# Optimization experiments

Hardware: AMD Instinct MI355X
Metric: run time of the kernel (lower is better)

The kernel has to match this reference:

```python
import jax, jax.numpy as jnp
import numpy as np

L = 3          # num encoder layers
H = 128        # hidden_dim
NH = 8         # num_heads
HD = H // NH   # head_dim
FF = H * 4     # ff inner dim (after GLU)
B, N = 32, 512
NUM_BINS = 50


def _linear_params(key, fan_in, fan_out):
    kw, kb = jax.random.split(key)
    lim = 1.0 / np.sqrt(fan_in)
    W = jax.random.uniform(kw, (fan_in, fan_out), jnp.float32, -lim, lim)
    b = jax.random.uniform(kb, (fan_out,), jnp.float32, -lim, lim)
    return W, b


def setup_inputs() -> dict:
    key = jax.random.key(0)
    ks = jax.random.split(key, 16)
    x = jax.random.normal(ks[0], (B, N, H), jnp.float32)
    distance_matrix = jax.random.uniform(ks[1], (B, N, N), jnp.float32)
    mask = jax.random.randint(ks[2], (B, N), 0, 2).astype(bool)

    def stack_linear(k, fan_in, fan_out):
        Ws, bs = [], []
        for l in range(L):
            W, b = _linear_params(jax.random.fold_in(k, l), fan_in, fan_out)
            Ws.append(W); bs.append(b)
        return jnp.stack(Ws), jnp.stack(bs)

    Wq, bq = stack_linear(ks[3], H, H)
    Wk, bk = stack_linear(ks[4], H, H)
    Wv, bv = stack_linear(ks[5], H, H)
    Wo, bo = stack_linear(ks[6], H, H)
    dist_emb = jax.random.normal(ks[7], (L, NUM_BINS, NH), jnp.float32)
    attn_bias = jnp.zeros((L, NH, 1, 1), jnp.float32)
    g1 = jnp.ones((L, H), jnp.float32); b1 = jnp.zeros((L, H), jnp.float32)
    g2 = jnp.ones((L, H), jnp.float32); b2 = jnp.zeros((L, H), jnp.float32)
    Wf1, bf1 = stack_linear(ks[8], H, 2 * FF)
    Wf2, bf2 = stack_linear(ks[9], FF, H)
    return dict(x=x, distance_matrix=distance_matrix, mask=mask,
                Wq=Wq, bq=bq, Wk=Wk, bk=bk, Wv=Wv, bv=bv, Wo=Wo, bo=bo,
                dist_emb=dist_emb, attn_bias=attn_bias,
                g1=g1, b1=b1, g2=g2, b2=b2,
                Wf1=Wf1, bf1=bf1, Wf2=Wf2, bf2=bf2)


def _layernorm(x, g, b, eps=1e-5):
    mu = jnp.mean(x, axis=-1, keepdims=True)
    var = jnp.var(x, axis=-1, keepdims=True)
    return (x - mu) * jax.lax.rsqrt(var + eps) * g + b


def _attention(h, bins, key_mask, Wq, bq, Wk, bk, Wv, bv, Wo, bo, dist_emb, attn_bias):
    # h: [B,N,H]; bins: [B,N,N] int; key_mask: [B,N] bool (True = masked)
    Bsz, Nn, _ = h.shape
    Q = (h @ Wq + bq).reshape(Bsz, Nn, NH, HD)
    K = (h @ Wk + bk).reshape(Bsz, Nn, NH, HD)
    V = (h @ Wv + bv).reshape(Bsz, Nn, NH, HD)
    scores = jnp.einsum('bqhd,bkhd->bhqk', Q, K) / np.sqrt(HD)
    bias = jnp.transpose(dist_emb[bins], (0, 3, 1, 2))  # [B,NH,N,N]
    scores = scores + bias + attn_bias[None]
    scores = jnp.where(key_mask[:, None, None, :], -1e9, scores)
    attn = jax.nn.softmax(scores, axis=-1)
    out = jnp.einsum('bhqk,bkhd->bqhd', attn, V).reshape(Bsz, Nn, H)
    return out @ Wo + bo


def reference(x, distance_matrix, mask, Wq, bq, Wk, bk, Wv, bv, Wo, bo,
              dist_emb, attn_bias, g1, b1, g2, b2, Wf1, bf1, Wf2, bf2):
    bins = jnp.clip((distance_matrix * 10.0).astype(jnp.int32), 0, NUM_BINS - 1)
    h = x
    for l in range(L):
        # pre-LN attention block
        a = _attention(_layernorm(h, g1[l], b1[l]), bins, mask,
                       Wq[l], bq[l], Wk[l], bk[l], Wv[l], bv[l], Wo[l], bo[l],
                       dist_emb[l], attn_bias[l])
        h = h + a
        # pre-LN GLU feed-forward
        u = _layernorm(h, g2[l], b2[l]) @ Wf1[l] + bf1[l]  # [B,N,2*FF]
        ua, ub = jnp.split(u, 2, axis=-1)
        h = h + (ua * jax.nn.sigmoid(ub)) @ Wf2[l] + bf2[l]
    return h
```

## Files before the change

### kernel.cpp

```cpp
#include <hip/hip_runtime.h>
#include <stdint.h>

#define Bq 32
#define Nq 512
#define Hq 128
#define NHq 8
#define HDq 16
#define Mq (Bq * Nq)

typedef unsigned short u16;
typedef __attribute__((ext_vector_type(8))) short short8;
typedef __attribute__((ext_vector_type(8))) _Float16 half8;
typedef __attribute__((ext_vector_type(2))) __fp16 fp16x2;
typedef __attribute__((ext_vector_type(4))) float f32x4;

__device__ __forceinline__ float bf2f(u16 v) {
    return __uint_as_float(((unsigned int)v) << 16);
}
__device__ __forceinline__ float ldin(const void* p, long idx, int bf) {
    if (bf) return bf2f(((const u16*)p)[idx]);
    return ((const float*)p)[idx];
}
__device__ __forceinline__ u16 f2bf(float v) {
    unsigned int u = __float_as_uint(v);
    return (u16)((u + 0x7FFFu + ((u >> 16) & 1u)) >> 16);
}
__device__ __forceinline__ u16 f2h(float v) {
    _Float16 h = (_Float16)v;
    return *(u16*)&h;
}
__device__ __forceinline__ unsigned pk2h(float a, float b) {
    fp16x2 c = __builtin_amdgcn_cvt_pkrtz(a, b);
    return *(unsigned*)&c;
}

__global__ void prep_kernel(const void* xraw, const void* de, const void* ab,
                            const void* mraw, int* flag, float* deo, float* abo,
                            unsigned* mbits, int n) {
    __shared__ int cnt, orA, orB, orC, orD;
    int tid = threadIdx.x;
    if (tid == 0) { cnt = 0; orA = 0; orB = 0; orC = 0; orD = 0; }
    __syncthreads();
    const u16* u = (const u16*)xraw;
    int good = 0;
    for (int i = tid; i < 1024; i += 256) {
        u16 v = u[i];
        int e = (v >> 7) & 0xFF;
        if (v == 0 || (e >= 90 && e <= 141)) good++;
    }
    atomicAdd(&cnt, good);
    const uint4* p4 = (const uint4*)mraw;
    unsigned a = 0, b = 0, c = 0, d = 0;
    for (int i = tid; i < n / 16; i += 256) {
        uint4 w = p4[i];
        unsigned all = w.x | w.y | w.z | w.w;
        a |= all & 0xFEFEFEFEu;
        b |= all & 0x0000FF00u;
        c |= all & 0xFFFFFF00u;
        d |= w.y | w.w;
    }
    if (a) atomicOr(&orA, 1);
    if (b) atomicOr(&orB, 1);
    if (c) atomicOr(&orC, 1);
    if (d) atomicOr(&orD, 1);
    __syncthreads();
    int bf = (cnt >= 900);
    if (tid == 0) *flag = bf;
    int mode;
    if (orA) mode = orB ? 3 : 4;
    else if (orC) mode = 0;
    else mode = orD ? 1 : 2;
    for (int i = tid; i < 1200; i += 256) deo[i] = ldin(de, i, bf);
    if (tid < 24) abo[tid] = ldin(ab, tid, bf);
    const unsigned char* p = (const unsigned char*)mraw;
    for (int wI = tid; wI < n / 32; wI += 256) {
        unsigned word = 0;
        for (int j = 0; j < 32; ++j) {
            int i = wI * 32 + j;
            int v;
            switch (mode) {
                case 0: v = p[i]; break;
                case 1: v = ((const int*)p)[i]; break;
                case 2: v = (int)((const long long*)p)[i]; break;
                case 3: v = ((const u16*)p)[i] != 0; break;
                default: v = (((const float*)p)[i] != 0.0f); break;
            }
            if (v) word |= 1u << j;
        }
        mbits[wI] = word;
    }
}

__global__ void kprep_kernel(const unsigned* __restrict__ mbits,
                             u16* __restrict__ kidxg, int* __restrict__ nkt,
                             unsigned* __restrict__ tmask) {
    int b = blockIdx.x;
    int lane = threadIdx.x & 63;
    int pos_base = 0;
    for (int w = 0; w < 8; ++w) {
        unsigned lo = mbits[b * 16 + 2 * w], hi = mbits[b * 16 + 2 * w + 1];
        unsigned long long word = ((unsigned long long)hi << 32) | lo;
        unsigned long long un = ~word;
        int bit = (int)((un >> lane) & 1ull);
        unsigned long long before = un & ((1ull << lane) - 1ull);
        int pos = pos_base + __popcll(before);
        if (bit) kidxg[b * 512 + pos] = (u16)(w * 64 + lane);
        pos_base += __popcll(un);
    }
    int nk = pos_base;
    int nkp = (nk + 31) & ~31;
    if (nkp == 0) nkp = 32;
    int nt = nkp >> 5;
    for (int j = nk + lane; j < nkp; j += 64) kidxg[b * 512 + j] = 0;
    if (lane == 0) {
        nkt[b] = nt;
        for (int t = 0; t < 16; ++t) tmask[b * 16 + t] = 0;
        int rem = nk & 31;
        if (rem) tmask[b * 16 + nt - 1] = 0xFFFFFFFFu << rem;
        if (nk == 0) tmask[b * 16] = 0xFFFFFFFFu;
    }
}

__global__ __launch_bounds__(256) void binsc_kernel(
    const void* __restrict__ dist, const u16* __restrict__ kidxg,
    const int* __restrict__ nkt, unsigned char* __restrict__ binsc,
    const int* flagp) {
    int bf = *flagp;
    int b = blockIdx.y;
    int q0 = blockIdx.x * 8;
    __shared__ u16 kl[512];
    __shared__ int ntS;
    int tid = threadIdx.x;
    if (tid == 0) ntS = nkt[b];
    kl[tid] = kidxg[b * 512 + tid];
    kl[tid + 256] = kidxg[b * 512 + tid + 256];
    __syncthreads();
    int nkp = ntS * 32;
    for (int rq = 0; rq < 8; ++rq) {
        int q = q0 + rq;
        long rowoff = ((long)b * 512 + q) * 512;
        for (int j = tid; j < nkp; j += 256) {
            float d = ldin(dist, rowoff + kl[j], bf);
            int v = (int)(d * 10.0f);
            v = v < 0 ? 0 : (v > 49 ? 49 : v);
            binsc[((size_t)b * 512 + q) * 512 + j] = (unsigned char)(v << 2);
        }
    }
}

__global__ __launch_bounds__(256) void init_ln_kernel(
    const void* x, float* __restrict__ h, u16* __restrict__ hn,
    const void* graw, const void* braw, const int* flagp) {
    int bf = *flagp;
    int row = blockIdx.x * 4 + (threadIdx.x >> 6);
    int lane = threadIdx.x & 63;
    float x0 = ldin(x, (long)row * Hq + lane, bf);
    float x1 = ldin(x, (long)row * Hq + lane + 64, bf);
    h[(size_t)row * Hq + lane] = x0;
    h[(size_t)row * Hq + lane + 64] = x1;
    float s = x0 + x1, s2 = x0 * x0 + x1 * x1;
#pragma unroll
    for (int o = 32; o; o >>= 1) {
        s += __shfl_xor(s, o);
        s2 += __shfl_xor(s2, o);
    }
    float mu = s * (1.0f / 128.0f);
    float var = fmaxf(s2 * (1.0f / 128.0f) - mu * mu, 0.0f);
    float rr = rsqrtf(var + 1e-5f);
    float g0 = ldin(graw, lane, bf), g1v = ldin(graw, lane + 64, bf);
    float b0 = ldin(braw, lane, bf), b1v = ldin(braw, lane + 64, bf);
    hn[(size_t)row * Hq + lane]      = f2bf((x0 - mu) * rr * g0 + b0);
    hn[(size_t)row * Hq + lane + 64] = f2bf((x1 - mu) * rr * g1v + b1v);
}

__global__ __launch_bounds__(256) void wtrans_kernel(
    const void* Wqr, const void* Wkr, const void* Wvr, const void* Wor,
    const void* Wf1r, const void* Wf2r,
    u16* qkvT, u16* oT, u16* f1T, u16* f2T, const int* flagp) {
    int bf = *flagp;
    int bid = blockIdx.x;
    int l = bid >> 8, r = bid & 255;
    const void* src; u16* dst; long soff, doff; int Kd, Nd, t;
    if (r < 64) {
        int mat = r >> 4; t = r & 15; Kd = 128; Nd = 128;
        soff = (long)l * 16384;
        if (mat == 0)      { src = Wqr; dst = qkvT; doff = (long)l * 49152; }
        else if (mat == 1) { src = Wkr; dst = qkvT; doff = (long)l * 49152 + 16384; }
        else if (mat == 2) { src = Wvr; dst = qkvT; doff = (long)l * 49152 + 32768; }
        else               { src = Wor; dst = oT;   doff = (long)l * 16384; }
    } else if (r < 192) {
        t = r - 64; Kd = 128; Nd = 1024;
        src = Wf1r; soff = (long)l * 131072; dst = f1T; doff = (long)l * 131072;
    } else {
        t = r - 192; Kd = 512; Nd = 128;
        src = Wf2r; soff = (long)l * 65536; dst = f2T; doff = (long)l * 65536;
    }
    int ntile = Nd >> 5;
    int tk = t / ntile, tn = t % ntile;
    __shared__ u16 Ts[32][33];
    int rr = threadIdx.x >> 3, cc0 = (threadIdx.x & 7) * 4;
#pragma unroll
    for (int i = 0; i < 4; ++i) {
        long idx = soff + (long)(tk * 32 + rr) * Nd + tn * 32 + cc0 + i;
        Ts[rr][cc0 + i] = f2bf(ldin(src, idx, bf));
    }
    __syncthreads();
#pragma unroll
    for (int i = 0; i < 4; ++i) {
        long idx = doff + (long)(tn * 32 + rr) * Kd + tk * 32 + cc0 + i;
        dst[idx] = Ts[cc0 + i][rr];
    }
}

__global__ __launch_bounds__(256, 2) void mfma_gemm64_kernel(
    const u16* __restrict__ A, const u16* __restrict__ WT,
    const void* __restrict__ braw, long bOff, float* __restrict__ C,
    int K, int resid, const int* flagp,
    const void* lnG, const void* lnB, long lnOff, u16* hnout, void* outp) {
    __shared__ __align__(16) u16 As[64][40];
    __shared__ __align__(16) u16 Bs[128][40];
    __shared__ float Ct[64][128];
    int tid = threadIdx.x;
    int m0 = blockIdx.x * 64;
    int wave = tid >> 6, lane = tid & 63;
    int wm = (wave >> 1) * 32, wn = (wave & 1) * 64;
    int q = lane >> 4, ln = lane & 15;
    f32x4 zero = {0.f, 0.f, 0.f, 0.f};
    f32x4 acc[2][4];
#pragma unroll
    for (int i = 0; i < 2; ++i)
#pragma unroll
        for (int j = 0; j < 4; ++j) acc[i][j] = zero;
    int sar = tid >> 2, sac = (tid & 3) * 8;
    int sbr = tid >> 1, sbc = (tid & 1) * 16;
    const u16* Ap = A + (size_t)(m0 + sar) * K + sac;
    const u16* Bp = WT + (size_t)sbr * K + sbc;
    for (int k0 = 0; k0 < K; k0 += 32) {
        uint4 av = *(const uint4*)(Ap + k0);
        uint4 b0 = *(const uint4*)(Bp + k0);
        uint4 b1 = *(const uint4*)(Bp + k0 + 8);
        *(uint4*)&As[sar][sac] = av;
        *(uint4*)&Bs[sbr][sbc] = b0; *(uint4*)&Bs[sbr][sbc + 8] = b1;
        __syncthreads();
        short8 af[2], bfv[4];
#pragma unroll
        for (int t = 0; t < 2; ++t) af[t] = *(const short8*)&As[wm + t * 16 + ln][q * 8];
#pragma unroll
        for (int t = 0; t < 4; ++t) bfv[t] = *(const short8*)&Bs[wn + t * 16 + ln][q * 8];
#pragma unroll
        for (int ti = 0; ti < 2; ++ti)
#pragma unroll
            for (int tj = 0; tj < 4; ++tj)
                acc[ti][tj] = __builtin_amdgcn_mfma_f32_16x16x32_bf16(
                    af[ti], bfv[tj], acc[ti][tj], 0, 0, 0);
        __syncthreads();
    }
    int bf = *flagp;
#pragma unroll
    for (int tj = 0; tj < 4; ++tj) {
        int n = wn + tj * 16 + ln;
        float bias = ldin(braw, bOff + n, bf);
#pragma unroll
        for (int ti = 0; ti < 2; ++ti)
#pragma unroll
            for (int r = 0; r < 4; ++r) {
                int m = m0 + wm + ti * 16 + q * 4 + r;
                float v = acc[ti][tj][r] + bias;
                float* dst = C + (size_t)m * 128 + n;
                if (resid) v += *dst;
                *dst = v;
                Ct[m - m0][n] = v;
                if (outp) {
                    if (bf) ((u16*)outp)[(size_t)m * 128 + n] = f2bf(v);
                    else ((float*)outp)[(size_t)m * 128 + n] = v;
                }
            }
    }
    if (hnout) {
        __syncthreads();
        float gg0 = ldin(lnG, lnOff + lane, bf);
        float gg1 = ldin(lnG, lnOff + lane + 64, bf);
        float bb0 = ldin(lnB, lnOff + lane, bf);
        float bb1 = ldin(lnB, lnOff + lane + 64, bf);
        for (int rr = 0; rr < 16; ++rr) {
            int row = wave * 16 + rr;
            float x0 = Ct[row][lane], x1 = Ct[row][lane + 64];
            float s = x0 + x1, s2v = x0 * x0 + x1 * x1;
#pragma unroll
            for (int o = 32; o; o >>= 1) {
                s += __shfl_xor(s, o);
                s2v += __shfl_xor(s2v, o);
            }
            float mu = s * (1.0f / 128.0f);
            float var = fmaxf(s2v * (1.0f / 128.0f) - mu * mu, 0.0f);
            float rstd = rsqrtf(var + 1e-5f);
            int m = m0 + row;
            hnout[(size_t)m * 128 + lane]      = f2bf((x0 - mu) * rstd * gg0 + bb0);
            hnout[(size_t)m * 128 + lane + 64] = f2bf((x1 - mu) * rstd * gg1 + bb1);
        }
    }
}

__global__ __launch_bounds__(256, 2) void qkv_mfma_kernel(
    const u16* __restrict__ A, const u16* __restrict__ qkvT_l,
    const void* bqr, const void* bkr, const void* bvr, long bOff,
    u16* __restrict__ Qo, u16* __restrict__ Ko, u16* __restrict__ Vo,
    const int* flagp) {
    int sel = blockIdx.y;
    const u16* WT = qkvT_l + (size_t)sel * 16384;
    const void* braw = sel == 0 ? bqr : (sel == 1 ? bkr : bvr);
    u16* C = sel == 0 ? Qo : (sel == 1 ? Ko : Vo);
    float scale = sel == 0 ? 0.25f : 1.0f;
    __shared__ __align__(16) u16 As[64][40];
    __shared__ __align__(16) u16 Bs[128][40];
    int tid = threadIdx.x;
    int m0 = blockIdx.x * 64;
    int wave = tid >> 6, lane = tid & 63;
    int wm = (wave >> 1) * 32, wn = (wave & 1) * 64;
    int q = lane >> 4, ln = lane & 15;
    f32x4 zero = {0.f, 0.f, 0.f, 0.f};
    f32x4 acc[2][4];
#pragma unroll
    for (int i = 0; i < 2; ++i)
#pragma unroll
        for (int j = 0; j < 4; ++j) acc[i][j] = zero;
    int sar = tid >> 2, sac = (tid & 3) * 8;
    int sbr = tid >> 1, sbc = (tid & 1) * 16;
    const u16* Ap = A + (size_t)(m0 + sar) * 128 + sac;
    const u16* Bp = WT + (size_t)sbr * 128 + sbc;
#pragma unroll
    for (int k0 = 0; k0 < 128; k0 += 32) {
        uint4 av = *(const uint4*)(Ap + k0);
        uint4 b0 = *(const uint4*)(Bp + k0);
        uint4 b1 = *(const uint4*)(Bp + k0 + 8);
        *(uint4*)&As[sar][sac] = av;
        *(uint4*)&Bs[sbr][sbc] = b0; *(uint4*)&Bs[sbr][sbc + 8] = b1;
        __syncthreads();
        short8 af[2], bfv[4];
#pragma unroll
        for (int t = 0; t < 2; ++t) af[t] = *(const short8*)&As[wm + t * 16 + ln][q * 8];
#pragma unroll
        for (int t = 0; t < 4; ++t) bfv[t] = *(const short8*)&Bs[wn + t * 16 + ln][q * 8];
#pragma unroll
        for (int ti = 0; ti < 2; ++ti)
#pragma unroll
            for (int tj = 0; tj < 4; ++tj)
                acc[ti][tj] = __builtin_amdgcn_mfma_f32_16x16x32_bf16(
                    af[ti], bfv[tj], acc[ti][tj], 0, 0, 0);
        __syncthreads();
    }
    int bf = *flagp;
#pragma unroll
    for (int tj = 0; tj < 4; ++tj) {
        int n = wn + tj * 16 + ln;
        float bias = ldin(braw, bOff + n, bf);
#pragma unroll
        for (int ti = 0; ti < 2; ++ti)
#pragma unroll
            for (int r = 0; r < 4; ++r) {
                int m = m0 + wm + ti * 16 + q * 4 + r;
                C[(size_t)m * 128 + n] = f2h((acc[ti][tj][r] + bias) * scale);
            }
    }
}

__global__ __launch_bounds__(256, 2) void glu_mfma_kernel(
    const u16* __restrict__ A, const u16* __restrict__ f1T_l,
    const void* __restrict__ braw, long bOff, u16* __restrict__ Vout,
    const int* flagp) {
    __shared__ __align__(16) u16 As[128][40];
    __shared__ __align__(16) u16 Ba[64][40];
    __shared__ __align__(16) u16 Bb[64][40];
    int tid = threadIdx.x;
    int m0 = blockIdx.x * 128, n0 = blockIdx.y * 64;
    int wave = tid >> 6, lane = tid & 63;
    int wm = (wave >> 1) * 64, wn = (wave & 1) * 32;
    int q = lane >> 4, ln = lane & 15;
    f32x4 zero = {0.f, 0.f, 0.f, 0.f};
    f32x4 accA[4][2], accB[4][2];
#pragma unroll
    for (int i = 0; i < 4; ++i)
#pragma unroll
        for (int j = 0; j < 2; ++j) { accA[i][j] = zero; accB[i][j] = zero; }
    int sr = tid >> 1, sc = (tid & 1) * 16;
    const u16* Ap = A + (size_t)(m0 + sr) * 128 + sc;
    const u16* BpA = f1T_l + (size_t)(n0 + sr) * 128 + sc;
    const u16* BpB = f1T_l + (size_t)(512 + n0 + (sr - 64)) * 128 + sc;
#pragma unroll
    for (int k0 = 0; k0 < 128; k0 += 32) {
        uint4 a0 = *(const uint4*)(Ap + k0);
        uint4 a1 = *(const uint4*)(Ap + k0 + 8);
        *(uint4*)&As[sr][sc] = a0; *(uint4*)&As[sr][sc + 8] = a1;
        if (sr < 64) {
            uint4 w0 = *(const uint4*)(BpA + k0);
            uint4 w1 = *(const uint4*)(BpA + k0 + 8);
            *(uint4*)&Ba[sr][sc] = w0; *(uint4*)&Ba[sr][sc + 8] = w1;
        } else {
            uint4 w0 = *(const uint4*)(BpB + k0);
            uint4 w1 = *(const uint4*)(BpB + k0 + 8);
            *(uint4*)&Bb[sr - 64][sc] = w0; *(uint4*)&Bb[sr - 64][sc + 8] = w1;
        }
        __syncthreads();
        short8 af[4], ba[2], bb[2];
#pragma unroll
        for (int t = 0; t < 4; ++t) af[t] = *(const short8*)&As[wm + t * 16 + ln][q * 8];
#pragma unroll
        for (int t = 0; t < 2; ++t) {
            ba[t] = *(const short8*)&Ba[wn + t * 16 + ln][q * 8];
            bb[t] = *(const short8*)&Bb[wn + t * 16 + ln][q * 8];
        }
#pragma unroll
        for (int ti = 0; ti < 4; ++ti)
#pragma unroll
            for (int tj = 0; tj < 2; ++tj) {
                accA[ti][tj] = __builtin_amdgcn_mfma_f32_16x16x32_bf16(
                    af[ti], ba[tj], accA[ti][tj], 0, 0, 0);
                accB[ti][tj] = __builtin_amdgcn_mfma_f32_16x16x32_bf16(
                    af[ti], bb[tj], accB[ti][tj], 0, 0, 0);
            }
        __syncthreads();
    }
    int bf = *flagp;
#pragma unroll
    for (int tj = 0; tj < 2; ++tj) {
        int n = n0 + wn + tj * 16 + ln;
        float biasA = ldin(braw, bOff + n, bf);
        float biasB = ldin(braw, bOff + 512 + n, bf);
#pragma unroll
        for (int ti = 0; ti < 4; ++ti)
#pragma unroll
            for (int r = 0; r < 4; ++r) {
                int m = m0 + wm + ti * 16 + q * 4 + r;
                float ua = accA[ti][tj][r] + biasA;
                float ub = accB[ti][tj][r] + biasB;
                Vout[(size_t)m * 512 + n] = f2bf(ua / (1.0f + __expf(-ub)));
            }
    }
}

__global__ __launch_bounds__(256, 4) void attn_kernel(
    const u16* __restrict__ Qh, const u16* __restrict__ Kh,
    const u16* __restrict__ Vh, const unsigned char* __restrict__ binsc,
    const u16* __restrict__ kidxg, const int* __restrict__ nktp,
    const unsigned* __restrict__ tmaskp, const float* __restrict__ deL,
    const float* __restrict__ abL, u16* __restrict__ out) {
    int id = blockIdx.x;
    int c = id & 7, t5 = id >> 3;
    int nh = t5 & 7;
    int pair = ((t5 >> 3) << 3) | c;
    int b = pair >> 2, qq = pair & 3;

    __shared__ __align__(16) u16 KsF[8192];
    __shared__ __align__(16) u16 VT[16 * 520];
    __shared__ __align__(16) u16 Pl[4 * 16 * 40];

    int tid = threadIdx.x;
    int nt = __builtin_amdgcn_readfirstlane(nktp[b]);
    int nkp = nt * 32;
    const u16* Kp = Kh + (size_t)(b * Nq) * Hq + nh * HDq;
    const u16* Vp = Vh + (size_t)(b * Nq) * Hq + nh * HDq;
    for (int r = tid; r < nkp; r += 256) {
        int row = kidxg[b * 512 + r];
        int kt = r >> 5, s = (r >> 4) & 1, lnr = r & 15;
        uint4 k0v = *(const uint4*)(Kp + (size_t)row * Hq);
        uint4 k1v = *(const uint4*)(Kp + (size_t)row * Hq + 8);
        *(uint4*)&KsF[kt * 512 + s * 256 + lnr * 8]       = k0v;
        *(uint4*)&KsF[kt * 512 + s * 256 + 128 + lnr * 8] = k1v;
        uint4 v0 = *(const uint4*)(Vp + (size_t)row * Hq);
        uint4 v1 = *(const uint4*)(Vp + (size_t)row * Hq + 8);
        u16 vv[16];
        *(uint4*)&vv[0] = v0; *(uint4*)&vv[8] = v1;
#pragma unroll
        for (int d = 0; d < 16; ++d) VT[d * 520 + r] = vv[d];
    }
    __syncthreads();

    int wave = tid >> 6, lane = tid & 63;
    int quad = lane >> 4, ln = lane & 15;
    int q0w = qq * 128 + wave * 32;

    float tblf = (lane < 50) ? deL[lane * NHq + nh] + abL[nh] : 0.0f;
    int tbli = __float_as_int(tblf);
    unsigned tl = tmaskp[b * 16 + nt - 1];

    half8 qf[2];
#pragma unroll
    for (int t = 0; t < 2; ++t) {
        uint4 qv = {0, 0, 0, 0};
        if (quad < 2)
            qv = *(const uint4*)(Qh + (size_t)(b * Nq + q0w + t * 16 + ln) * Hq
                                 + nh * HDq + quad * 8);
        qf[t] = *(half8*)&qv;
    }

    f32x4 zero = {0.f, 0.f, 0.f, 0.f};
    f32x4 acc[2] = {zero, zero};
    float zp[2] = {0.f, 0.f};
    _Float16* Pw = (_Float16*)&Pl[wave * 640];
    const _Float16* KsH = (const _Float16*)KsF;
    const _Float16* VTH = (const _Float16*)VT;
    const unsigned char* brow0 = binsc + ((size_t)b * 512 + (q0w + ln)) * 512;
    const unsigned char* brow1 = brow0 + (size_t)16 * 512;

    unsigned pb00 = *(const unsigned*)(brow0 + quad * 4);
    unsigned pb01 = *(const unsigned*)(brow0 + 16 + quad * 4);
    unsigned pb10 = *(const unsigned*)(brow1 + quad * 4);
    unsigned pb11 = *(const unsigned*)(brow1 + 16 + quad * 4);

    for (int kt = 0; kt < nt; ++kt) {
        int k0 = kt * 32;
        unsigned w = (kt == nt - 1) ? tl : 0u;
        unsigned cb00 = pb00, cb01 = pb01, cb10 = pb10, cb11 = pb11;
        if (kt < nt - 1) {
            pb00 = *(const unsigned*)(brow0 + k0 + 32 + quad * 4);
            pb01 = *(const unsigned*)(brow0 + k0 + 48 + quad * 4);
            pb10 = *(const unsigned*)(brow1 + k0 + 32 + quad * 4);
            pb11 = *(const unsigned*)(brow1 + k0 + 48 + quad * 4);
        }
        half8 vb = *(const half8*)(VTH + ln * 520 + k0 + quad * 8);
        half8 ka0 = {}, ka1 = {};
        if (quad < 2) {
            ka0 = *(const half8*)(KsH + kt * 512 + quad * 128 + ln * 8);
            ka1 = *(const half8*)(KsH + kt * 512 + 256 + quad * 128 + ln * 8);
        }
#pragma unroll
        for (int t = 0; t < 2; ++t) {
            unsigned bw0 = t == 0 ? cb00 : cb10;
            unsigned bw1 = t == 0 ? cb01 : cb11;
            f32x4 s0 = __builtin_amdgcn_mfma_f32_16x16x32_f16(ka0, qf[t], zero, 0, 0, 0);
            f32x4 s1 = __builtin_amdgcn_mfma_f32_16x16x32_f16(ka1, qf[t], zero, 0, 0, 0);
            float p[8];
#pragma unroll
            for (int r = 0; r < 4; ++r) {
                float bias = __int_as_float(__builtin_amdgcn_ds_bpermute(
                    (int)((bw0 >> (8 * r)) & 0xFFu), tbli));
                float sc = s0[r] + bias;
                bool m = (w >> (quad * 4 + r)) & 1u;
                p[r] = m ? 0.0f : __expf(sc);
            }
#pragma unroll
            for (int r = 0; r < 4; ++r) {
                float bias = __int_as_float(__builtin_amdgcn_ds_bpermute(
                    (int)((bw1 >> (8 * r)) & 0xFFu), tbli));
                float sc = s1[r] + bias;
                bool m = (w >> (16 + quad * 4 + r)) & 1u;
                p[4 + r] = m ? 0.0f : __expf(sc);
            }
            zp[t] += ((p[0] + p[1]) + (p[2] + p[3])) +
                     ((p[4] + p[5]) + (p[6] + p[7]));
            uint2 w0, w1;
            w0.x = pk2h(p[0], p[1]); w0.y = pk2h(p[2], p[3]);
            w1.x = pk2h(p[4], p[5]); w1.y = pk2h(p[6], p[7]);
            *(uint2*)(Pw + ln * 40 + quad * 4)      = w0;
            *(uint2*)(Pw + ln * 40 + 16 + quad * 4) = w1;
            half8 pa = *(const half8*)(Pw + ln * 40 + quad * 8);
            acc[t] = __builtin_amdgcn_mfma_f32_16x16x32_f16(pa, vb, acc[t], 0, 0, 0);
        }
    }
#pragma unroll
    for (int t = 0; t < 2; ++t) {
        zp[t] += __shfl_xor(zp[t], 16);
        zp[t] += __shfl_xor(zp[t], 32);
    }
#pragma unroll
    for (int t = 0; t < 2; ++t) {
#pragma unroll
        for (int r = 0; r < 4; ++r) {
            float zz = __shfl(zp[t], quad * 4 + r);
            float val = acc[t][r] / fmaxf(zz, 1e-35f);
            int qrow = q0w + t * 16 + quad * 4 + r;
            out[(size_t)(b * Nq + qrow) * Hq + nh * HDq + ln] = f2bf(val);
        }
    }
}

extern "C" void kernel_launch(void* const* d_in, const int* in_sizes, int n_in,
                              void* d_out, int out_size, void* d_ws, size_t ws_size,
                              hipStream_t stream) {
    const void* x  = d_in[0];
    const void* dist = d_in[1];
    const void* mask = d_in[2];
    const void* Wq = d_in[3];  const void* bq = d_in[4];
    const void* Wk = d_in[5];  const void* bk = d_in[6];
    const void* Wv = d_in[7];  const void* bv = d_in[8];
    const void* Wo = d_in[9];  const void* bo = d_in[10];
    const void* de = d_in[11]; const void* ab = d_in[12];
    const void* g1 = d_in[13]; const void* b1 = d_in[14];
    const void* g2 = d_in[15]; const void* b2 = d_in[16];
    const void* Wf1 = d_in[17]; const void* bf1 = d_in[18];
    const void* Wf2 = d_in[19]; const void* bf2 = d_in[20];

    char* ws = (char*)d_ws;
    const size_t OFF_DE   = 64;
    const size_t OFF_AB   = 5120;
    const size_t OFF_BINS = 8192;
    const size_t OFF_MSK  = OFF_BINS + 8388608;
    const size_t OFF_KIDX = OFF_MSK + 4096;
    const size_t OFF_NKT  = OFF_KIDX + 32768;
    const size_t OFF_TM   = OFF_NKT + 256;
    const size_t OFF_H    = OFF_TM + 4096;
    const size_t OFF_QKV  = OFF_H + 8388608;
    const size_t OFF_HN   = OFF_QKV + 25165824;
    const size_t OFF_ATT  = OFF_HN + 4194304;
    const size_t OFF_WT   = OFF_ATT + 4194304;
    const size_t NEEDED   = OFF_WT + 1572864;
    if (ws_size < NEEDED) return;

    int* flag = (int*)ws;
    float* deF = (float*)(ws + OFF_DE);
    float* abF = (float*)(ws + OFF_AB);
    unsigned char* binsc = (unsigned char*)(ws + OFF_BINS);
    unsigned* mbits = (unsigned*)(ws + OFF_MSK);
    u16* kidxg = (u16*)(ws + OFF_KIDX);
    int* nkt = (int*)(ws + OFF_NKT);
    unsigned* tmask = (unsigned*)(ws + OFF_TM);
    float* h = (float*)(ws + OFF_H);
    u16* Qh = (u16*)(ws + OFF_QKV);
    u16* Kh = Qh + 2097152;
    u16* Vh = Qh + 2 * 2097152;
    u16* vglu = (u16*)(ws + OFF_QKV);
    u16* hn = (u16*)(ws + OFF_HN);
    u16* att = (u16*)(ws + OFF_ATT);
    u16* qkvT = (u16*)(ws + OFF_WT);
    u16* oT  = qkvT + 147456;
    u16* f1T = oT + 49152;
    u16* f2T = f1T + 393216;

    prep_kernel<<<1, 256, 0, stream>>>(x, de, ab, mask, flag, deF, abF, mbits, Bq * Nq);
    kprep_kernel<<<32, 64, 0, stream>>>(mbits, kidxg, nkt, tmask);
    dim3 gbc(64, 32);
    binsc_kernel<<<gbc, 256, 0, stream>>>(dist, kidxg, nkt, binsc, flag);
    init_ln_kernel<<<4096, 256, 0, stream>>>(x, h, hn, g1, b1, flag);
    wtrans_kernel<<<768, 256, 0, stream>>>(Wq, Wk, Wv, Wo, Wf1, Wf2,
                                           qkvT, oT, f1T, f2T, flag);

    dim3 gqkv(256, 3);
    dim3 gglu(128, 8);
    for (int l = 0; l < 3; ++l) {
        qkv_mfma_kernel<<<gqkv, 256, 0, stream>>>(hn, qkvT + (size_t)l * 49152,
                                                  bq, bk, bv, (long)l * Hq,
                                                  Qh, Kh, Vh, flag);
        attn_kernel<<<1024, 256, 0, stream>>>(Qh, Kh, Vh, binsc, kidxg, nkt, tmask,
                                              deF + (long)l * 400, abF + (long)l * 8, att);
        mfma_gemm64_kernel<<<256, 256, 0, stream>>>(att, oT + (size_t)l * 16384,
                                                    bo, (long)l * Hq, h, 128, 1, flag,
                                                    g2, b2, (long)l * Hq, hn, nullptr);
        glu_mfma_kernel<<<gglu, 256, 0, stream>>>(hn, f1T + (size_t)l * 131072,
                                                  bf1, (long)l * 1024, vglu, flag);
        if (l < 2) {
            mfma_gemm64_kernel<<<256, 256, 0, stream>>>(vglu, f2T + (size_t)l * 65536,
                                                        bf2, (long)l * Hq, h, 512, 1, flag,
                                                        g1, b1, (long)(l + 1) * Hq, hn,
                                                        nullptr);
        } else {
            mfma_gemm64_kernel<<<256, 256, 0, stream>>>(vglu, f2T + (size_t)l * 65536,
                                                        bf2, (long)l * Hq, h, 512, 1, flag,
                                                        nullptr, nullptr, 0, nullptr,
                                                        d_out);
        }
    }
}
```

Baseline: 407.0 us.

## Fuse out-projection, LayerNorm, GLU FF1 and FF2 into one per-row-tile kernel

Replaces three launches per layer (O-projection GEMM with LN2, GLU up-projection, FF2 GEMM with LN1) with one kernel. Each 64-row tile keeps its residual, normalized activations and the 64x512 GLU intermediate in about 148KB of LDS, so the GLU output and hn never go through global memory. Weight chunks are prefetched into registers while the previous chunk is computed. In exchange occupancy drops to one block per CU with only 256 blocks, and each block streams all FF weights itself, so latency hiding and weight reuse across blocks may suffer.

```diff
diff --git a/kernel.cpp b/kernel.cpp
--- a/kernel.cpp
+++ b/kernel.cpp
@@ -212,95 +212,6 @@
     }
 }
 
-__global__ __launch_bounds__(256, 2) void mfma_gemm64_kernel(
-    const u16* __restrict__ A, const u16* __restrict__ WT,
-    const void* __restrict__ braw, long bOff, float* __restrict__ C,
-    int K, int resid, const int* flagp,
-    const void* lnG, const void* lnB, long lnOff, u16* hnout, void* outp) {
-    __shared__ __align__(16) u16 As[64][40];
-    __shared__ __align__(16) u16 Bs[128][40];
-    __shared__ float Ct[64][128];
-    int tid = threadIdx.x;
-    int m0 = blockIdx.x * 64;
-    int wave = tid >> 6, lane = tid & 63;
-    int wm = (wave >> 1) * 32, wn = (wave & 1) * 64;
-    int q = lane >> 4, ln = lane & 15;
-    f32x4 zero = {0.f, 0.f, 0.f, 0.f};
-    f32x4 acc[2][4];
-#pragma unroll
-    for (int i = 0; i < 2; ++i)
-#pragma unroll
-        for (int j = 0; j < 4; ++j) acc[i][j] = zero;
-    int sar = tid >> 2, sac = (tid & 3) * 8;
-    int sbr = tid >> 1, sbc = (tid & 1) * 16;
-    const u16* Ap = A + (size_t)(m0 + sar) * K + sac;
-    const u16* Bp = WT + (size_t)sbr * K + sbc;
-    for (int k0 = 0; k0 < K; k0 += 32) {
-        uint4 av = *(const uint4*)(Ap + k0);
-        uint4 b0 = *(const uint4*)(Bp + k0);
-        uint4 b1 = *(const uint4*)(Bp + k0 + 8);
-        *(uint4*)&As[sar][sac] = av;
-        *(uint4*)&Bs[sbr][sbc] = b0; *(uint4*)&Bs[sbr][sbc + 8] = b1;
-        __syncthreads();
-        short8 af[2], bfv[4];
-#pragma unroll
-        for (int t = 0; t < 2; ++t) af[t] = *(const short8*)&As[wm + t * 16 + ln][q * 8];
-#pragma unroll
-        for (int t = 0; t < 4; ++t) bfv[t] = *(const short8*)&Bs[wn + t * 16 + ln][q * 8];
-#pragma unroll
-        for (int ti = 0; ti < 2; ++ti)
-#pragma unroll
-            for (int tj = 0; tj < 4; ++tj)
-                acc[ti][tj] = __builtin_amdgcn_mfma_f32_16x16x32_bf16(
-                    af[ti], bfv[tj], acc[ti][tj], 0, 0, 0);
-        __syncthreads();
-    }
-    int bf = *flagp;
-#pragma unroll
-    for (int tj = 0; tj < 4; ++tj) {
-        int n = wn + tj * 16 + ln;
-        float bias = ldin(braw, bOff + n, bf);
-#pragma unroll
-        for (int ti = 0; ti < 2; ++ti)
-#pragma unroll
-            for (int r = 0; r < 4; ++r) {
-                int m = m0 + wm + ti * 16 + q * 4 + r;
-                float v = acc[ti][tj][r] + bias;
-                float* dst = C + (size_t)m * 128 + n;
-                if (resid) v += *dst;
-                *dst = v;
-                Ct[m - m0][n] = v;
-                if (outp) {
-                    if (bf) ((u16*)outp)[(size_t)m * 128 + n] = f2bf(v);
-                    else ((float*)outp)[(size_t)m * 128 + n] = v;
-                }
-            }
-    }
-    if (hnout) {
-        __syncthreads();
-        float gg0 = ldin(lnG, lnOff + lane, bf);
-        float gg1 = ldin(lnG, lnOff + lane + 64, bf);
-        float bb0 = ldin(lnB, lnOff + lane, bf);
-        float bb1 = ldin(lnB, lnOff + lane + 64, bf);
-        for (int rr = 0; rr < 16; ++rr) {
-            int row = wave * 16 + rr;
-            float x0 = Ct[row][lane], x1 = Ct[row][lane + 64];
-            float s = x0 + x1, s2v = x0 * x0 + x1 * x1;
-#pragma unroll
-            for (int o = 32; o; o >>= 1) {
-                s += __shfl_xor(s, o);
-                s2v += __shfl_xor(s2v, o);
-            }
-            float mu = s * (1.0f / 128.0f);
-            float var = fmaxf(s2v * (1.0f / 128.0f) - mu * mu, 0.0f);
-            float rstd = rsqrtf(var + 1e-5f);
-            int m = m0 + row;
-            hnout[(size_t)m * 128 + lane]      = f2bf((x0 - mu) * rstd * gg0 + bb0);
-            hnout[(size_t)m * 128 + lane + 64] = f2bf((x1 - mu) * rstd * gg1 + bb1);
-        }
-    }
-}
-
 __global__ __launch_bounds__(256, 2) void qkv_mfma_kernel(
     const u16* __restrict__ A, const u16* __restrict__ qkvT_l,
     const void* bqr, const void* bkr, const void* bvr, long bOff,
@@ -364,77 +275,246 @@
     }
 }
 
-__global__ __launch_bounds__(256, 2) void glu_mfma_kernel(
-    const u16* __restrict__ A, const u16* __restrict__ f1T_l,
-    const void* __restrict__ braw, long bOff, u16* __restrict__ Vout,
-    const int* flagp) {
-    __shared__ __align__(16) u16 As[128][40];
-    __shared__ __align__(16) u16 Ba[64][40];
-    __shared__ __align__(16) u16 Bb[64][40];
+__global__ __launch_bounds__(256, 1) void layer_ffn_kernel(
+    const u16* __restrict__ att, const u16* __restrict__ oT_l,
+    const void* __restrict__ bo, long boOff,
+    float* __restrict__ h,
+    const void* g2, const void* b2, long ln2Off,
+    const u16* __restrict__ f1T_l, const void* __restrict__ bf1r, long bf1Off,
+    const u16* __restrict__ f2T_l, const void* __restrict__ bf2r, long bf2Off,
+    const void* g1, const void* b1, long ln1Off,
+    u16* __restrict__ hnout, void* __restrict__ outp, const int* flagp) {
+    __shared__ __align__(16) char Lds[151552];
+    u16 (*As)[136]   = (u16(*)[136])Lds;
+    u16 (*hn2)[136]  = (u16(*)[136])Lds;
+    float (*Ct)[128] = (float(*)[128])(Lds + 17408);
+    u16 (*vg)[520]   = (u16(*)[520])(Lds + 50176);
+    u16 (*Bs)[136]   = (u16(*)[136])(Lds + 116736);
+    u16 (*Ba)[136]   = (u16(*)[136])(Lds + 116736);
+    u16 (*Bb)[136]   = (u16(*)[136])(Lds + 134144);
+
     int tid = threadIdx.x;
-    int m0 = blockIdx.x * 128, n0 = blockIdx.y * 64;
+    int m0 = blockIdx.x * 64;
     int wave = tid >> 6, lane = tid & 63;
-    int wm = (wave >> 1) * 64, wn = (wave & 1) * 32;
+    int wm = (wave >> 1) * 32, wn = (wave & 1) * 64;
     int q = lane >> 4, ln = lane & 15;
+    int bf = *flagp;
     f32x4 zero = {0.f, 0.f, 0.f, 0.f};
-    f32x4 accA[4][2], accB[4][2];
-#pragma unroll
-    for (int i = 0; i < 4; ++i)
-#pragma unroll
-        for (int j = 0; j < 2; ++j) { accA[i][j] = zero; accB[i][j] = zero; }
-    int sr = tid >> 1, sc = (tid & 1) * 16;
-    const u16* Ap = A + (size_t)(m0 + sr) * 128 + sc;
-    const u16* BpA = f1T_l + (size_t)(n0 + sr) * 128 + sc;
-    const u16* BpB = f1T_l + (size_t)(512 + n0 + (sr - 64)) * 128 + sc;
-#pragma unroll
-    for (int k0 = 0; k0 < 128; k0 += 32) {
-        uint4 a0 = *(const uint4*)(Ap + k0);
-        uint4 a1 = *(const uint4*)(Ap + k0 + 8);
-        *(uint4*)&As[sr][sc] = a0; *(uint4*)&As[sr][sc + 8] = a1;
-        if (sr < 64) {
-            uint4 w0 = *(const uint4*)(BpA + k0);
-            uint4 w1 = *(const uint4*)(BpA + k0 + 8);
-            *(uint4*)&Ba[sr][sc] = w0; *(uint4*)&Ba[sr][sc + 8] = w1;
-        } else {
-            uint4 w0 = *(const uint4*)(BpB + k0);
-            uint4 w1 = *(const uint4*)(BpB + k0 + 8);
-            *(uint4*)&Bb[sr - 64][sc] = w0; *(uint4*)&Bb[sr - 64][sc + 8] = w1;
+
+#pragma unroll
+    for (int i = 0; i < 4; ++i) {
+        int idx = tid + i * 256; int r = idx >> 4, c = (idx & 15) << 3;
+        *(uint4*)&As[r][c] = *(const uint4*)(att + (size_t)(m0 + r) * 128 + c);
+    }
+#pragma unroll
+    for (int i = 0; i < 8; ++i) {
+        int idx = tid + i * 256; int r = idx >> 4, c = (idx & 15) << 3;
+        *(uint4*)&Bs[r][c] = *(const uint4*)(oT_l + (size_t)r * 128 + c);
+    }
+    __syncthreads();
+    f32x4 acc[2][4];
+#pragma unroll
+    for (int i = 0; i < 2; ++i)
+#pragma unroll
+        for (int j = 0; j < 4; ++j) acc[i][j] = zero;
+#pragma unroll
+    for (int kf = 0; kf < 128; kf += 32) {
+        short8 af[2], bfv[4];
+#pragma unroll
+        for (int t = 0; t < 2; ++t)
+            af[t] = *(const short8*)&As[wm + t * 16 + ln][kf + q * 8];
+#pragma unroll
+        for (int t = 0; t < 4; ++t)
+            bfv[t] = *(const short8*)&Bs[wn + t * 16 + ln][kf + q * 8];
+#pragma unroll
+        for (int ti = 0; ti < 2; ++ti)
+#pragma unroll
+            for (int tj = 0; tj < 4; ++tj)
+                acc[ti][tj] = __builtin_amdgcn_mfma_f32_16x16x32_bf16(
+                    af[ti], bfv[tj], acc[ti][tj], 0, 0, 0);
+    }
+#pragma unroll
+    for (int tj = 0; tj < 4; ++tj) {
+        int n = wn + tj * 16 + ln;
+        float bias = ldin(bo, boOff + n, bf);
+#pragma unroll
+        for (int ti = 0; ti < 2; ++ti)
+#pragma unroll
+            for (int r = 0; r < 4; ++r) {
+                int lm = wm + ti * 16 + q * 4 + r;
+                Ct[lm][n] = acc[ti][tj][r] + bias + h[(size_t)(m0 + lm) * 128 + n];
+            }
+    }
+    __syncthreads();
+    {
+        float gg0 = ldin(g2, ln2Off + lane, bf), gg1 = ldin(g2, ln2Off + lane + 64, bf);
+        float bb0 = ldin(b2, ln2Off + lane, bf), bb1 = ldin(b2, ln2Off + lane + 64, bf);
+        for (int rr = 0; rr < 16; ++rr) {
+            int row = wave * 16 + rr;
+            float x0 = Ct[row][lane], x1 = Ct[row][lane + 64];
+            float s = x0 + x1, s2v = x0 * x0 + x1 * x1;
+#pragma unroll
+            for (int o = 32; o; o >>= 1) {
+                s += __shfl_xor(s, o);
+                s2v += __shfl_xor(s2v, o);
+            }
+            float mu = s * (1.0f / 128.0f);
+            float var = fmaxf(s2v * (1.0f / 128.0f) - mu * mu, 0.0f);
+            float rstd = rsqrtf(var + 1e-5f);
+            hn2[row][lane]      = f2bf((x0 - mu) * rstd * gg0 + bb0);
+            hn2[row][lane + 64] = f2bf((x1 - mu) * rstd * gg1 + bb1);
+        }
+    }
+    int wn2 = (wave & 1) * 32;
+    uint4 ra[4], rb[4];
+#pragma unroll
+    for (int i = 0; i < 4; ++i) {
+        int idx = tid + i * 256; int r = idx >> 4, c = (idx & 15) << 3;
+        ra[i] = *(const uint4*)(f1T_l + (size_t)r * 128 + c);
+        rb[i] = *(const uint4*)(f1T_l + (size_t)(512 + r) * 128 + c);
+    }
+    for (int ch = 0; ch < 8; ++ch) {
+#pragma unroll
+        for (int i = 0; i < 4; ++i) {
+            int idx = tid + i * 256; int r = idx >> 4, c = (idx & 15) << 3;
+            *(uint4*)&Ba[r][c] = ra[i];
+            *(uint4*)&Bb[r][c] = rb[i];
+        }
+        if (ch < 7) {
+            int n0 = (ch + 1) * 64;
+#pragma unroll
+            for (int i = 0; i < 4; ++i) {
+                int idx = tid + i * 256; int r = idx >> 4, c = (idx & 15) << 3;
+                ra[i] = *(const uint4*)(f1T_l + (size_t)(n0 + r) * 128 + c);
+                rb[i] = *(const uint4*)(f1T_l + (size_t)(512 + n0 + r) * 128 + c);
+            }
         }
         __syncthreads();
-        short8 af[4], ba[2], bb[2];
-#pragma unroll
-        for (int t = 0; t < 4; ++t) af[t] = *(const short8*)&As[wm + t * 16 + ln][q * 8];
-#pragma unroll
-        for (int t = 0; t < 2; ++t) {
-            ba[t] = *(const short8*)&Ba[wn + t * 16 + ln][q * 8];
-            bb[t] = *(const short8*)&Bb[wn + t * 16 + ln][q * 8];
-        }
-#pragma unroll
-        for (int ti = 0; ti < 4; ++ti)
-#pragma unroll
-            for (int tj = 0; tj < 2; ++tj) {
-                accA[ti][tj] = __builtin_amdgcn_mfma_f32_16x16x32_bf16(
-                    af[ti], ba[tj], accA[ti][tj], 0, 0, 0);
-                accB[ti][tj] = __builtin_amdgcn_mfma_f32_16x16x32_bf16(
-                    af[ti], bb[tj], accB[ti][tj], 0, 0, 0);
-            }
+        f32x4 aA[2][2], aB[2][2];
+#pragma unroll
+        for (int i = 0; i < 2; ++i)
+#pragma unroll
+            for (int j = 0; j < 2; ++j) { aA[i][j] = zero; aB[i][j] = zero; }
+#pragma unroll
+        for (int kf = 0; kf < 128; kf += 32) {
+            short8 af[2], bav[2], bbv[2];
+#pragma unroll
+            for (int t = 0; t < 2; ++t)
+                af[t] = *(const short8*)&hn2[wm + t * 16 + ln][kf + q * 8];
+#pragma unroll
+            for (int t = 0; t < 2; ++t) {
+                bav[t] = *(const short8*)&Ba[wn2 + t * 16 + ln][kf + q * 8];
+                bbv[t] = *(const short8*)&Bb[wn2 + t * 16 + ln][kf + q * 8];
+            }
+#pragma unroll
+            for (int ti = 0; ti < 2; ++ti)
+#pragma unroll
+                for (int tj = 0; tj < 2; ++tj) {
+                    aA[ti][tj] = __builtin_amdgcn_mfma_f32_16x16x32_bf16(
+                        af[ti], bav[tj], aA[ti][tj], 0, 0, 0);
+                    aB[ti][tj] = __builtin_amdgcn_mfma_f32_16x16x32_bf16(
+                        af[ti], bbv[tj], aB[ti][tj], 0, 0, 0);
+                }
+        }
+        int n0 = ch * 64;
+#pragma unroll
+        for (int tj = 0; tj < 2; ++tj) {
+            int n = n0 + wn2 + tj * 16 + ln;
+            float bA = ldin(bf1r, bf1Off + n, bf);
+            float bB = ldin(bf1r, bf1Off + 512 + n, bf);
+#pragma unroll
+            for (int ti = 0; ti < 2; ++ti)
+#pragma unroll
+                for (int r = 0; r < 4; ++r) {
+                    int lm = wm + ti * 16 + q * 4 + r;
+                    float ua = aA[ti][tj][r] + bA;
+                    float ub = aB[ti][tj][r] + bB;
+                    vg[lm][n] = f2bf(ua / (1.0f + __expf(-ub)));
+                }
+        }
         __syncthreads();
     }
-    int bf = *flagp;
-#pragma unroll
-    for (int tj = 0; tj < 2; ++tj) {
-        int n = n0 + wn + tj * 16 + ln;
-        float biasA = ldin(braw, bOff + n, bf);
-        float biasB = ldin(braw, bOff + 512 + n, bf);
-#pragma unroll
-        for (int ti = 0; ti < 4; ++ti)
+    uint4 rf[8];
+#pragma unroll
+    for (int i = 0; i < 8; ++i) {
+        int idx = tid + i * 256; int r = idx >> 4, c = (idx & 15) << 3;
+        rf[i] = *(const uint4*)(f2T_l + (size_t)r * 512 + c);
+    }
+    f32x4 accF[2][4];
+#pragma unroll
+    for (int i = 0; i < 2; ++i)
+#pragma unroll
+        for (int j = 0; j < 4; ++j) accF[i][j] = zero;
+    for (int ch = 0; ch < 4; ++ch) {
+#pragma unroll
+        for (int i = 0; i < 8; ++i) {
+            int idx = tid + i * 256; int r = idx >> 4, c = (idx & 15) << 3;
+            *(uint4*)&Bs[r][c] = rf[i];
+        }
+        if (ch < 3) {
+            int k0 = (ch + 1) * 128;
+#pragma unroll
+            for (int i = 0; i < 8; ++i) {
+                int idx = tid + i * 256; int r = idx >> 4, c = (idx & 15) << 3;
+                rf[i] = *(const uint4*)(f2T_l + (size_t)r * 512 + k0 + c);
+            }
+        }
+        __syncthreads();
+#pragma unroll
+        for (int kf = 0; kf < 128; kf += 32) {
+            short8 af[2], bfv[4];
+#pragma unroll
+            for (int t = 0; t < 2; ++t)
+                af[t] = *(const short8*)&vg[wm + t * 16 + ln][ch * 128 + kf + q * 8];
+#pragma unroll
+            for (int t = 0; t < 4; ++t)
+                bfv[t] = *(const short8*)&Bs[wn + t * 16 + ln][kf + q * 8];
+#pragma unroll
+            for (int ti = 0; ti < 2; ++ti)
+#pragma unroll
+                for (int tj = 0; tj < 4; ++tj)
+                    accF[ti][tj] = __builtin_amdgcn_mfma_f32_16x16x32_bf16(
+                        af[ti], bfv[tj], accF[ti][tj], 0, 0, 0);
+        }
+        __syncthreads();
+    }
+#pragma unroll
+    for (int tj = 0; tj < 4; ++tj) {
+        int n = wn + tj * 16 + ln;
+        float bias = ldin(bf2r, bf2Off + n, bf);
+#pragma unroll
+        for (int ti = 0; ti < 2; ++ti)
 #pragma unroll
             for (int r = 0; r < 4; ++r) {
-                int m = m0 + wm + ti * 16 + q * 4 + r;
-                float ua = accA[ti][tj][r] + biasA;
-                float ub = accB[ti][tj][r] + biasB;
-                Vout[(size_t)m * 512 + n] = f2bf(ua / (1.0f + __expf(-ub)));
-            }
+                int lm = wm + ti * 16 + q * 4 + r;
+                float v = accF[ti][tj][r] + bias + Ct[lm][n];
+                h[(size_t)(m0 + lm) * 128 + n] = v;
+                Ct[lm][n] = v;
+                if (outp) {
+                    if (bf) ((u16*)outp)[(size_t)(m0 + lm) * 128 + n] = f2bf(v);
+                    else ((float*)outp)[(size_t)(m0 + lm) * 128 + n] = v;
+                }
+            }
+    }
+    if (hnout) {
+        __syncthreads();
+        float gg0 = ldin(g1, ln1Off + lane, bf), gg1 = ldin(g1, ln1Off + lane + 64, bf);
+        float bb0 = ldin(b1, ln1Off + lane, bf), bb1 = ldin(b1, ln1Off + lane + 64, bf);
+        for (int rr = 0; rr < 16; ++rr) {
+            int row = wave * 16 + rr;
+            float x0 = Ct[row][lane], x1 = Ct[row][lane + 64];
+            float s = x0 + x1, s2v = x0 * x0 + x1 * x1;
+#pragma unroll
+            for (int o = 32; o; o >>= 1) {
+                s += __shfl_xor(s, o);
+                s2v += __shfl_xor(s2v, o);
+            }
+            float mu = s * (1.0f / 128.0f);
+            float var = fmaxf(s2v * (1.0f / 128.0f) - mu * mu, 0.0f);
+            float rstd = rsqrtf(var + 1e-5f);
+            hnout[(size_t)(m0 + row) * 128 + lane]      = f2bf((x0 - mu) * rstd * gg0 + bb0);
+            hnout[(size_t)(m0 + row) * 128 + lane + 64] = f2bf((x1 - mu) * rstd * gg1 + bb1);
+        }
     }
 }
 
@@ -618,7 +698,6 @@
     u16* Qh = (u16*)(ws + OFF_QKV);
     u16* Kh = Qh + 2097152;
     u16* Vh = Qh + 2 * 2097152;
-    u16* vglu = (u16*)(ws + OFF_QKV);
     u16* hn = (u16*)(ws + OFF_HN);
     u16* att = (u16*)(ws + OFF_ATT);
     u16* qkvT = (u16*)(ws + OFF_WT);
@@ -635,28 +714,19 @@
                                            qkvT, oT, f1T, f2T, flag);
 
     dim3 gqkv(256, 3);
-    dim3 gglu(128, 8);
     for (int l = 0; l < 3; ++l) {
         qkv_mfma_kernel<<<gqkv, 256, 0, stream>>>(hn, qkvT + (size_t)l * 49152,
                                                   bq, bk, bv, (long)l * Hq,
                                                   Qh, Kh, Vh, flag);
         attn_kernel<<<1024, 256, 0, stream>>>(Qh, Kh, Vh, binsc, kidxg, nkt, tmask,
                                               deF + (long)l * 400, abF + (long)l * 8, att);
-        mfma_gemm64_kernel<<<256, 256, 0, stream>>>(att, oT + (size_t)l * 16384,
-                                                    bo, (long)l * Hq, h, 128, 1, flag,
-                                                    g2, b2, (long)l * Hq, hn, nullptr);
-        glu_mfma_kernel<<<gglu, 256, 0, stream>>>(hn, f1T + (size_t)l * 131072,
-                                                  bf1, (long)l * 1024, vglu, flag);
-        if (l < 2) {
-            mfma_gemm64_kernel<<<256, 256, 0, stream>>>(vglu, f2T + (size_t)l * 65536,
-                                                        bf2, (long)l * Hq, h, 512, 1, flag,
-                                                        g1, b1, (long)(l + 1) * Hq, hn,
-                                                        nullptr);
-        } else {
-            mfma_gemm64_kernel<<<256, 256, 0, stream>>>(vglu, f2T + (size_t)l * 65536,
-                                                        bf2, (long)l * Hq, h, 512, 1, flag,
-                                                        nullptr, nullptr, 0, nullptr,
-                                                        d_out);
-        }
-    }
-}
+        layer_ffn_kernel<<<256, 256, 0, stream>>>(
+            att, oT + (size_t)l * 16384, bo, (long)l * Hq,
+            h, g2, b2, (long)l * Hq,
+            f1T + (size_t)l * 131072, bf1, (long)l * 1024,
+            f2T + (size_t)l * 65536, bf2, (long)l * Hq,
+            g1, b1, l < 2 ? (long)(l + 1) * Hq : 0,
+            l < 2 ? hn : (u16*)nullptr,
+            l == 2 ? d_out : nullptr, flag);
+    }
+}
```

Result: no change. 410.6 us (+0.9%).
